# Performance work log

Measured on AMD Instinct MI355X. Metric: run time of the kernel, lower is better.

The kernel has to match this reference:

```python
import jax, jax.numpy as jnp
import numpy as np

CUTOFF = 5.0
COULOMB_CONSTANT = 14.3996454784936  # eV * Angstrom / e^2
SQRT2 = 1.4142135623730951
N_NODES = 500000
N_EDGES = 16000000


def polynomial_cutoff(r, cutoff):
    ratio = r / cutoff
    f = 1.0 - 6.0 * ratio**5 + 15.0 * ratio**4 - 10.0 * ratio**3
    return jnp.where(r <= cutoff, f, 0.0)


def setup_inputs() -> dict:
    key = jax.random.key(0)
    k1, k2, k3, k4, k5 = jax.random.split(key, 5)
    charge = jax.random.normal(k1, (N_NODES,), dtype=jnp.float32)
    # sigma in (0.5, 1.5): positive Gaussian widths
    sigma = jax.random.uniform(k2, (N_NODES,), dtype=jnp.float32) + 0.5
    # bond_dist in (0.1, CUTOFF)
    bond_dist = jax.random.uniform(k3, (N_EDGES,), dtype=jnp.float32) * (CUTOFF - 0.1) + 0.1
    src = jax.random.randint(k4, (N_EDGES,), 0, N_NODES, dtype=jnp.int32)
    dst = jax.random.randint(k5, (N_EDGES,), 0, N_NODES, dtype=jnp.int32)
    return {"charge": charge, "sigma": sigma, "bond_dist": bond_dist, "src": src, "dst": dst}


def reference(charge, sigma, bond_dist, src, dst):
    # Edge-wise message: q_dst * erf(r / (sqrt2 * gamma)) * fcut(r) / r * K
    gamma = jnp.sqrt(sigma[src] ** 2 + sigma[dst] ** 2)  # [E]
    msg = (
        charge[dst]
        * jax.scipy.special.erf(bond_dist / (SQRT2 * gamma))
        * polynomial_cutoff(bond_dist, CUTOFF)
        / bond_dist
    ) * COULOMB_CONSTANT
    # Sum-aggregate messages at destination nodes (DGL fn.sum semantics)
    elec_pot = jax.ops.segment_sum(msg, dst, num_segments=charge.shape[0])
    return elec_pot
```

## Files before the change

kernel.cpp:

```cpp
#include <hip/hip_runtime.h>
#include <hip/hip_fp16.h>
#include <math.h>
#include <stdint.h>

#define CUTOFF_F     5.0f
#define INV_CUTOFF   0.2f
#define KCOUL        14.3996454784936f
#define INV_SQRT2    0.7071067811865475f

typedef int            vint4    __attribute__((ext_vector_type(4)));
typedef float          vfloat4  __attribute__((ext_vector_type(4)));
typedef uint32_t       vuint4   __attribute__((ext_vector_type(4)));
typedef unsigned short vushort8 __attribute__((ext_vector_type(8)));

#define WSHIFT        11
#define WINDOW        2048
#define NB            245
#define EPT           8
#define EPB           4096
#define OFFS_STRIDE   256
#define SPAN_MAX      512

__device__ __forceinline__ float erf_approx(float x) {
    const float a1 = 0.254829592f, a2 = -0.284496736f, a3 = 1.421413741f,
                a4 = -1.453152027f, a5 = 1.061405429f, p = 0.3275911f;
    float t = __builtin_amdgcn_rcpf(fmaf(p, x, 1.0f));
    float poly = t * fmaf(t, fmaf(t, fmaf(t, fmaf(t, a5, a4), a3), a2), a1);
    return 1.0f - poly * __expf(-x * x);
}

__device__ __forceinline__ float edge_val(float rr, float s2sum) {
    float inv_gamma = rsqrtf(s2sum);
    float x  = rr * INV_CUTOFF;
    float fc = fmaf(x * x * x, fmaf(x, fmaf(-6.0f, x, 15.0f), -10.0f), 1.0f);
    fc = (rr <= CUTOFF_F) ? fc : 0.0f;
    return erf_approx(rr * INV_SQRT2 * inv_gamma) * fc * KCOUL
         * __builtin_amdgcn_rcpf(rr);
}

__global__ __launch_bounds__(256, 4) void p1_bin(
    const float* __restrict__ bond,
    const int*   __restrict__ src,
    const int*   __restrict__ dst,
    unsigned short* __restrict__ offs,
    uint32_t*       __restrict__ sl_out,
    unsigned short* __restrict__ r_out,
    int n_edges)
{
    __shared__ uint32_t hist[NB];
    __shared__ uint32_t scan_s[NB + 1];
    __shared__ alignas(16) uint32_t       buf_sl[EPB];
    __shared__ alignas(16) unsigned short buf_r[EPB];

    const int tid = threadIdx.x;
    const int e0  = blockIdx.x * EPB;

    if (tid < NB) hist[tid] = 0;
    __syncthreads();

    uint32_t slA[EPT], brA[EPT], slB[EPT], brB[EPT];
    unsigned short hrA[EPT], hrB[EPT];

    const bool full = (e0 + EPB <= n_edges);
    if (full) {
        {
            const vint4*   dp = (const vint4*)(dst + e0) + tid;
            const vint4*   sp = (const vint4*)(src + e0) + tid;
            const vfloat4* rp = (const vfloat4*)(bond + e0) + tid;
            vint4   d0 = __builtin_nontemporal_load(dp);
            vint4   d1 = __builtin_nontemporal_load(dp + 256);
            vint4   s0 = __builtin_nontemporal_load(sp);
            vint4   s1 = __builtin_nontemporal_load(sp + 256);
            vfloat4 r0 = __builtin_nontemporal_load(rp);
            vfloat4 r1 = __builtin_nontemporal_load(rp + 256);
            int   d[EPT] = {d0.x,d0.y,d0.z,d0.w,d1.x,d1.y,d1.z,d1.w};
            int   s[EPT] = {s0.x,s0.y,s0.z,s0.w,s1.x,s1.y,s1.z,s1.w};
            float r[EPT] = {r0.x,r0.y,r0.z,r0.w,r1.x,r1.y,r1.z,r1.w};
            #pragma unroll
            for (int j = 0; j < EPT; ++j) {
                unsigned b = (unsigned)d[j] >> WSHIFT;
                uint32_t rk = atomicAdd(&hist[b], 1u);
                brA[j] = (b << 16) | rk;
                slA[j] = ((uint32_t)s[j] << WSHIFT) | ((unsigned)d[j] & (WINDOW - 1));
                hrA[j] = __half_as_ushort(__float2half_rn(r[j]));
            }
        }
        {
            const vint4*   dp = (const vint4*)(dst + e0) + tid;
            const vint4*   sp = (const vint4*)(src + e0) + tid;
            const vfloat4* rp = (const vfloat4*)(bond + e0) + tid;
            vint4   d2 = __builtin_nontemporal_load(dp + 512);
            vint4   d3 = __builtin_nontemporal_load(dp + 768);
            vint4   s2 = __builtin_nontemporal_load(sp + 512);
            vint4   s3 = __builtin_nontemporal_load(sp + 768);
            vfloat4 r2 = __builtin_nontemporal_load(rp + 512);
            vfloat4 r3 = __builtin_nontemporal_load(rp + 768);
            int   d[EPT] = {d2.x,d2.y,d2.z,d2.w,d3.x,d3.y,d3.z,d3.w};
            int   s[EPT] = {s2.x,s2.y,s2.z,s2.w,s3.x,s3.y,s3.z,s3.w};
            float r[EPT] = {r2.x,r2.y,r2.z,r2.w,r3.x,r3.y,r3.z,r3.w};
            #pragma unroll
            for (int j = 0; j < EPT; ++j) {
                unsigned b = (unsigned)d[j] >> WSHIFT;
                uint32_t rk = atomicAdd(&hist[b], 1u);
                brB[j] = (b << 16) | rk;
                slB[j] = ((uint32_t)s[j] << WSHIFT) | ((unsigned)d[j] & (WINDOW - 1));
                hrB[j] = __half_as_ushort(__float2half_rn(r[j]));
            }
        }
    } else {
        #pragma unroll
        for (int j = 0; j < EPT; ++j) {
            int eA = e0 + (j >> 2) * 1024 + tid * 4 + (j & 3);
            int eB = eA + 2048;
            if (eA < n_edges) {
                int dv = dst[eA]; int sv = src[eA]; float rv = bond[eA];
                unsigned b = (unsigned)dv >> WSHIFT;
                uint32_t rk = atomicAdd(&hist[b], 1u);
                brA[j] = (b << 16) | rk;
                slA[j] = ((uint32_t)sv << WSHIFT) | ((unsigned)dv & (WINDOW - 1));
                hrA[j] = __half_as_ushort(__float2half_rn(rv));
            } else brA[j] = 0xFFFFFFFFu;
            if (eB < n_edges) {
                int dv = dst[eB]; int sv = src[eB]; float rv = bond[eB];
                unsigned b = (unsigned)dv >> WSHIFT;
                uint32_t rk = atomicAdd(&hist[b], 1u);
                brB[j] = (b << 16) | rk;
                slB[j] = ((uint32_t)sv << WSHIFT) | ((unsigned)dv & (WINDOW - 1));
                hrB[j] = __half_as_ushort(__float2half_rn(rv));
            } else brB[j] = 0xFFFFFFFFu;
        }
    }
    __syncthreads();

    if (tid < 64) {
        const int base = tid * 4;
        uint32_t v[4]; uint32_t s = 0;
        #pragma unroll
        for (int j = 0; j < 4; ++j) { v[j] = (base + j < NB) ? hist[base + j] : 0u; s += v[j]; }
        uint32_t inc = s;
        #pragma unroll
        for (int d = 1; d < 64; d <<= 1) {
            uint32_t up = __shfl_up(inc, d, 64);
            if (tid >= d) inc += up;
        }
        uint32_t excl = inc - s;
        #pragma unroll
        for (int j = 0; j < 4; ++j) {
            if (base + j <= NB) scan_s[base + j] = excl;
            excl += v[j];
        }
    }
    __syncthreads();

    #pragma unroll
    for (int j = 0; j < EPT; ++j)
        if (brA[j] != 0xFFFFFFFFu) {
            uint32_t p = scan_s[brA[j] >> 16] + (brA[j] & 0xFFFFu);
            buf_sl[p] = slA[j]; buf_r[p] = hrA[j];
        }
    #pragma unroll
    for (int j = 0; j < EPT; ++j)
        if (brB[j] != 0xFFFFFFFFu) {
            uint32_t p = scan_s[brB[j] >> 16] + (brB[j] & 0xFFFFu);
            buf_sl[p] = slB[j]; buf_r[p] = hrB[j];
        }
    __syncthreads();

    if (tid <= NB)
        offs[(size_t)blockIdx.x * OFFS_STRIDE + tid] = (unsigned short)scan_s[tid];

    {
        const vuint4* bs = (const vuint4*)buf_sl;
        vuint4* os = (vuint4*)(sl_out + (size_t)blockIdx.x * EPB);
        #pragma unroll
        for (int i = 0; i < EPB / 4 / 256; ++i)
            __builtin_nontemporal_store(bs[tid + i * 256], os + tid + i * 256);
        const vushort8* br = (const vushort8*)buf_r;
        vushort8* orr = (vushort8*)(r_out + (size_t)blockIdx.x * EPB);
        #pragma unroll
        for (int i = 0; i < EPB / 8 / 256; ++i)
            __builtin_nontemporal_store(br[tid + i * 256], orr + tid + i * 256);
    }
}

template<int WPB>
__global__ __launch_bounds__(256, 4) void p2_acc(
    const uint32_t*       __restrict__ sl_in,
    const unsigned short* __restrict__ r_in,
    const unsigned short* __restrict__ offs,
    const float*          __restrict__ sigma,
    float*                __restrict__ partials,
    int n_nodes, int nblk)
{
    __shared__ float acc[WINDOW];
    __shared__ float sig[WINDOW];
    __shared__ unsigned short offLo[SPAN_MAX];
    __shared__ uint32_t cum[SPAN_MAX + 1];

    const int g = blockIdx.x;
    const int b = g / WPB;
    const int w = g % WPB;

    vfloat4* accv = (vfloat4*)acc;
    for (int i = threadIdx.x; i < WINDOW / 4; i += 256)
        accv[i] = (vfloat4){0.f, 0.f, 0.f, 0.f};

    const int nbase  = b << WSHIFT;
    const int nvalid = (n_nodes - nbase < WINDOW) ? (n_nodes - nbase) : WINDOW;
    if (nvalid == WINDOW) {
        vfloat4* sv = (vfloat4*)sig;
        const vfloat4* gp = (const vfloat4*)(sigma + nbase);
        for (int i = threadIdx.x; i < WINDOW / 4; i += 256) sv[i] = gp[i];
    } else {
        for (int i = threadIdx.x; i < WINDOW; i += 256)
            sig[i] = (i < nvalid) ? sigma[nbase + i] : 0.f;
    }

    const int span = (nblk + WPB - 1) / WPB;
    const int blk0 = w * span;
    int blkN = nblk - blk0;
    if (blkN > span) blkN = span;
    if (blkN < 0) blkN = 0;
    for (int i = threadIdx.x; i < blkN; i += 256) {
        size_t o = (size_t)(blk0 + i) * OFFS_STRIDE + b;
        unsigned short lo = offs[o];
        offLo[i] = lo;
        cum[i] = (uint32_t)offs[o + 1] - lo;
    }
    __syncthreads();

    if (threadIdx.x < 64) {
        const int base = threadIdx.x * 8;
        uint32_t v[8]; uint32_t s = 0;
        #pragma unroll
        for (int j = 0; j < 8; ++j) { v[j] = (base + j < blkN) ? cum[base + j] : 0u; s += v[j]; }
        uint32_t inc = s;
        #pragma unroll
        for (int d = 1; d < 64; d <<= 1) {
            uint32_t up = __shfl_up(inc, d, 64);
            if (threadIdx.x >= d) inc += up;
        }
        uint32_t excl = inc - s;
        #pragma unroll
        for (int j = 0; j < 8; ++j) { uint32_t t = v[j]; cum[base + j] = excl; excl += t; }
        if (threadIdx.x == 63) cum[SPAN_MAX] = inc;
    }
    __syncthreads();

    const int wave = threadIdx.x >> 6, lane = threadIdx.x & 63;
    const uint32_t T = cum[blkN];

    const uint32_t chunk = (T + 3) >> 2;
    const uint32_t f0    = (uint32_t)wave * chunk;
    uint32_t fend        = f0 + chunk;
    if (fend > T) fend = T;

    if (f0 < fend) {
        int l = 0, r = blkN;
        while (l < r) {
            int m = (l + r) >> 1;
            if (cum[m + 1] <= f0) l = m + 1; else r = m;
        }
        int i = l;

        for (uint32_t fb = f0; fb < fend; fb += 64) {
            uint32_t f = fb + lane;
            int ii = i;
            if (f < fend) {
                while (cum[ii + 1] <= f) ++ii;
                uint32_t k = f - cum[ii];
                size_t addr = (size_t)(blk0 + ii) * EPB + offLo[ii] + k;
                uint32_t sl = sl_in[addr];
                float rr = __half2float(__ushort_as_half(r_in[addr]));
                float ss = sigma[sl >> WSHIFT];
                float sd = sig[sl & (WINDOW - 1)];
                float v  = edge_val(rr, fmaf(ss, ss, sd * sd));
                atomicAdd(&acc[sl & (WINDOW - 1)], v);
            }
            i = __shfl(ii, 63);
        }
    }
    __syncthreads();

    vfloat4* outp = (vfloat4*)(partials + (size_t)g * WINDOW);
    for (int i = threadIdx.x; i < WINDOW / 4; i += 256)
        __builtin_nontemporal_store(accv[i], outp + i);
}

template<int WPB>
__global__ __launch_bounds__(256) void p3_reduce(
    const float* __restrict__ partials,
    const float* __restrict__ charge,
    float*       __restrict__ out, int n_nodes)
{
    int n = blockIdx.x * 256 + threadIdx.x;
    if (n >= n_nodes) return;
    unsigned b     = (unsigned)n >> WSHIFT;
    unsigned local = (unsigned)n & (WINDOW - 1);
    const float* p = partials + ((size_t)b * WPB) * WINDOW + local;
    float sum = 0.0f;
    #pragma unroll
    for (int w = 0; w < WPB; ++w)
        sum += __builtin_nontemporal_load(p + (size_t)w * WINDOW);
    out[n] = charge[n] * sum;
}

__global__ __launch_bounds__(256) void edge_msg_atomic(
    const float* __restrict__ charge, const float* __restrict__ sigma,
    const float* __restrict__ bond, const int* __restrict__ src,
    const int* __restrict__ dst, float* __restrict__ out, int n_edges)
{
    int i = blockIdx.x * blockDim.x + threadIdx.x;
    if (i < n_edges) {
        float ss = sigma[src[i]], sd = sigma[dst[i]];
        float msg = charge[dst[i]] * edge_val(bond[i], fmaf(ss, ss, sd * sd));
        atomicAdd(&out[dst[i]], msg);
    }
}

extern "C" void kernel_launch(void* const* d_in, const int* in_sizes, int n_in,
                              void* d_out, int out_size, void* d_ws, size_t ws_size,
                              hipStream_t stream) {
    const float* charge = (const float*)d_in[0];
    const float* sigma  = (const float*)d_in[1];
    const float* bond   = (const float*)d_in[2];
    const int*   src    = (const int*)d_in[3];
    const int*   dst    = (const int*)d_in[4];
    float* out = (float*)d_out;

    int n_nodes = in_sizes[0];
    int n_edges = in_sizes[2];

    int nblk = (n_edges + EPB - 1) / EPB;

    size_t offs_b = (size_t)nblk * OFFS_STRIDE * sizeof(unsigned short);
    size_t sl_b   = (size_t)nblk * EPB * sizeof(uint32_t);
    size_t r_b    = (size_t)nblk * EPB * sizeof(unsigned short);
    size_t base_b = offs_b + sl_b + r_b;

    int wpb = 0;
    {
        size_t p16 = (size_t)NB * 16 * WINDOW * sizeof(float);
        size_t p8  = (size_t)NB * 8  * WINDOW * sizeof(float);
        int span16 = (nblk + 15) / 16, span8 = (nblk + 7) / 8;
        if (base_b + p16 <= ws_size && span16 <= SPAN_MAX) wpb = 16;
        else if (base_b + p8 <= ws_size && span8 <= SPAN_MAX) wpb = 8;
    }

    if (n_nodes <= NB * WINDOW && wpb != 0) {
        unsigned short* offs = (unsigned short*)d_ws;
        uint32_t*       slp  = (uint32_t*)((char*)d_ws + offs_b);
        unsigned short* rp   = (unsigned short*)((char*)d_ws + offs_b + sl_b);
        float* partial = (float*)((char*)d_ws + base_b);

        p1_bin<<<nblk, 256, 0, stream>>>(bond, src, dst, offs, slp, rp, n_edges);
        int blocks3 = (n_nodes + 255) / 256;
        if (wpb == 16) {
            p2_acc<16><<<NB * 16, 256, 0, stream>>>(slp, rp, offs, sigma, partial,
                                                    n_nodes, nblk);
            p3_reduce<16><<<blocks3, 256, 0, stream>>>(partial, charge, out, n_nodes);
        } else {
            p2_acc<8><<<NB * 8, 256, 0, stream>>>(slp, rp, offs, sigma, partial,
                                                  n_nodes, nblk);
            p3_reduce<8><<<blocks3, 256, 0, stream>>>(partial, charge, out, n_nodes);
        }
    } else {
        (void)hipMemsetAsync(out, 0, (size_t)n_nodes * sizeof(float), stream);
        int blocks = (n_edges + 255) / 256;
        edge_msg_atomic<<<blocks, 256, 0, stream>>>(charge, sigma, bond, src, dst,
                                                    out, n_edges);
    }
}
```

Baseline: 327.6 us.

## Compute edge messages in binning pass and store packed fp16 value records

The edge message (erf, cutoff, 1/r) is now computed in the binning kernel, which gathers sigma for both src and dst there. Each edge is stored as a single 32-bit record holding the local dst index and the message in fp16, replacing the separate src/dst word and fp16 distance. The accumulate kernel no longer loads sigma windows or does random sigma[src] gathers; it only reads records and does LDS atomics. This cuts intermediate traffic and p2's scattered gathers, at the cost of random dst-sigma gathers in p1 and fp16 rounding of the message value instead of the distance.

```diff
diff --git a/kernel.cpp b/kernel.cpp
--- a/kernel.cpp
+++ b/kernel.cpp
@@ -11,7 +11,6 @@
 typedef int            vint4    __attribute__((ext_vector_type(4)));
 typedef float          vfloat4  __attribute__((ext_vector_type(4)));
 typedef uint32_t       vuint4   __attribute__((ext_vector_type(4)));
-typedef unsigned short vushort8 __attribute__((ext_vector_type(8)));
 
 #define WSHIFT        11
 #define WINDOW        2048
@@ -38,19 +37,30 @@
          * __builtin_amdgcn_rcpf(rr);
 }
 
+__device__ __forceinline__ void pack_edge(
+    int dv, int sv_unused, float rv, float ss, float sd,
+    uint32_t* hist, uint32_t& br, uint32_t& rec)
+{
+    unsigned b = (unsigned)dv >> WSHIFT;
+    uint32_t rk = atomicAdd(&hist[b], 1u);
+    br = (b << 16) | rk;
+    float v = edge_val(rv, fmaf(ss, ss, sd * sd));
+    rec = ((uint32_t)((unsigned)dv & (WINDOW - 1)) << 16)
+        | (uint32_t)__half_as_ushort(__float2half_rn(v));
+}
+
 __global__ __launch_bounds__(256, 4) void p1_bin(
     const float* __restrict__ bond,
     const int*   __restrict__ src,
     const int*   __restrict__ dst,
+    const float* __restrict__ sigma,
     unsigned short* __restrict__ offs,
-    uint32_t*       __restrict__ sl_out,
-    unsigned short* __restrict__ r_out,
+    uint32_t*       __restrict__ rec_out,
     int n_edges)
 {
     __shared__ uint32_t hist[NB];
     __shared__ uint32_t scan_s[NB + 1];
-    __shared__ alignas(16) uint32_t       buf_sl[EPB];
-    __shared__ alignas(16) unsigned short buf_r[EPB];
+    __shared__ alignas(16) uint32_t buf[EPB];
 
     const int tid = threadIdx.x;
     const int e0  = blockIdx.x * EPB;
@@ -58,8 +68,7 @@
     if (tid < NB) hist[tid] = 0;
     __syncthreads();
 
-    uint32_t slA[EPT], brA[EPT], slB[EPT], brB[EPT];
-    unsigned short hrA[EPT], hrB[EPT];
+    uint32_t recA[EPT], brA[EPT], recB[EPT], brB[EPT];
 
     const bool full = (e0 + EPB <= n_edges);
     if (full) {
@@ -76,14 +85,12 @@
             int   d[EPT] = {d0.x,d0.y,d0.z,d0.w,d1.x,d1.y,d1.z,d1.w};
             int   s[EPT] = {s0.x,s0.y,s0.z,s0.w,s1.x,s1.y,s1.z,s1.w};
             float r[EPT] = {r0.x,r0.y,r0.z,r0.w,r1.x,r1.y,r1.z,r1.w};
+            float ss[EPT], sd[EPT];
             #pragma unroll
-            for (int j = 0; j < EPT; ++j) {
-                unsigned b = (unsigned)d[j] >> WSHIFT;
-                uint32_t rk = atomicAdd(&hist[b], 1u);
-                brA[j] = (b << 16) | rk;
-                slA[j] = ((uint32_t)s[j] << WSHIFT) | ((unsigned)d[j] & (WINDOW - 1));
-                hrA[j] = __half_as_ushort(__float2half_rn(r[j]));
-            }
+            for (int j = 0; j < EPT; ++j) { ss[j] = sigma[s[j]]; sd[j] = sigma[d[j]]; }
+            #pragma unroll
+            for (int j = 0; j < EPT; ++j)
+                pack_edge(d[j], s[j], r[j], ss[j], sd[j], hist, brA[j], recA[j]);
         }
         {
             const vint4*   dp = (const vint4*)(dst + e0) + tid;
@@ -98,14 +105,12 @@
             int   d[EPT] = {d2.x,d2.y,d2.z,d2.w,d3.x,d3.y,d3.z,d3.w};
             int   s[EPT] = {s2.x,s2.y,s2.z,s2.w,s3.x,s3.y,s3.z,s3.w};
             float r[EPT] = {r2.x,r2.y,r2.z,r2.w,r3.x,r3.y,r3.z,r3.w};
+            float ss[EPT], sd[EPT];
             #pragma unroll
-            for (int j = 0; j < EPT; ++j) {
-                unsigned b = (unsigned)d[j] >> WSHIFT;
-                uint32_t rk = atomicAdd(&hist[b], 1u);
-                brB[j] = (b << 16) | rk;
-                slB[j] = ((uint32_t)s[j] << WSHIFT) | ((unsigned)d[j] & (WINDOW - 1));
-                hrB[j] = __half_as_ushort(__float2half_rn(r[j]));
-            }
+            for (int j = 0; j < EPT; ++j) { ss[j] = sigma[s[j]]; sd[j] = sigma[d[j]]; }
+            #pragma unroll
+            for (int j = 0; j < EPT; ++j)
+                pack_edge(d[j], s[j], r[j], ss[j], sd[j], hist, brB[j], recB[j]);
         }
     } else {
         #pragma unroll
@@ -114,19 +119,11 @@
             int eB = eA + 2048;
             if (eA < n_edges) {
                 int dv = dst[eA]; int sv = src[eA]; float rv = bond[eA];
-                unsigned b = (unsigned)dv >> WSHIFT;
-                uint32_t rk = atomicAdd(&hist[b], 1u);
-                brA[j] = (b << 16) | rk;
-                slA[j] = ((uint32_t)sv << WSHIFT) | ((unsigned)dv & (WINDOW - 1));
-                hrA[j] = __half_as_ushort(__float2half_rn(rv));
+                pack_edge(dv, sv, rv, sigma[sv], sigma[dv], hist, brA[j], recA[j]);
             } else brA[j] = 0xFFFFFFFFu;
             if (eB < n_edges) {
                 int dv = dst[eB]; int sv = src[eB]; float rv = bond[eB];
-                unsigned b = (unsigned)dv >> WSHIFT;
-                uint32_t rk = atomicAdd(&hist[b], 1u);
-                brB[j] = (b << 16) | rk;
-                slB[j] = ((uint32_t)sv << WSHIFT) | ((unsigned)dv & (WINDOW - 1));
-                hrB[j] = __half_as_ushort(__float2half_rn(rv));
+                pack_edge(dv, sv, rv, sigma[sv], sigma[dv], hist, brB[j], recB[j]);
             } else brB[j] = 0xFFFFFFFFu;
         }
     }
@@ -154,46 +151,34 @@
 
     #pragma unroll
     for (int j = 0; j < EPT; ++j)
-        if (brA[j] != 0xFFFFFFFFu) {
-            uint32_t p = scan_s[brA[j] >> 16] + (brA[j] & 0xFFFFu);
-            buf_sl[p] = slA[j]; buf_r[p] = hrA[j];
-        }
+        if (brA[j] != 0xFFFFFFFFu)
+            buf[scan_s[brA[j] >> 16] + (brA[j] & 0xFFFFu)] = recA[j];
     #pragma unroll
     for (int j = 0; j < EPT; ++j)
-        if (brB[j] != 0xFFFFFFFFu) {
-            uint32_t p = scan_s[brB[j] >> 16] + (brB[j] & 0xFFFFu);
-            buf_sl[p] = slB[j]; buf_r[p] = hrB[j];
-        }
+        if (brB[j] != 0xFFFFFFFFu)
+            buf[scan_s[brB[j] >> 16] + (brB[j] & 0xFFFFu)] = recB[j];
     __syncthreads();
 
     if (tid <= NB)
         offs[(size_t)blockIdx.x * OFFS_STRIDE + tid] = (unsigned short)scan_s[tid];
 
     {
-        const vuint4* bs = (const vuint4*)buf_sl;
-        vuint4* os = (vuint4*)(sl_out + (size_t)blockIdx.x * EPB);
+        const vuint4* bs = (const vuint4*)buf;
+        vuint4* os = (vuint4*)(rec_out + (size_t)blockIdx.x * EPB);
         #pragma unroll
         for (int i = 0; i < EPB / 4 / 256; ++i)
             __builtin_nontemporal_store(bs[tid + i * 256], os + tid + i * 256);
-        const vushort8* br = (const vushort8*)buf_r;
-        vushort8* orr = (vushort8*)(r_out + (size_t)blockIdx.x * EPB);
-        #pragma unroll
-        for (int i = 0; i < EPB / 8 / 256; ++i)
-            __builtin_nontemporal_store(br[tid + i * 256], orr + tid + i * 256);
     }
 }
 
 template<int WPB>
 __global__ __launch_bounds__(256, 4) void p2_acc(
-    const uint32_t*       __restrict__ sl_in,
-    const unsigned short* __restrict__ r_in,
+    const uint32_t*       __restrict__ rec_in,
     const unsigned short* __restrict__ offs,
-    const float*          __restrict__ sigma,
     float*                __restrict__ partials,
     int n_nodes, int nblk)
 {
     __shared__ float acc[WINDOW];
-    __shared__ float sig[WINDOW];
     __shared__ unsigned short offLo[SPAN_MAX];
     __shared__ uint32_t cum[SPAN_MAX + 1];
 
@@ -204,17 +189,6 @@
     vfloat4* accv = (vfloat4*)acc;
     for (int i = threadIdx.x; i < WINDOW / 4; i += 256)
         accv[i] = (vfloat4){0.f, 0.f, 0.f, 0.f};
-
-    const int nbase  = b << WSHIFT;
-    const int nvalid = (n_nodes - nbase < WINDOW) ? (n_nodes - nbase) : WINDOW;
-    if (nvalid == WINDOW) {
-        vfloat4* sv = (vfloat4*)sig;
-        const vfloat4* gp = (const vfloat4*)(sigma + nbase);
-        for (int i = threadIdx.x; i < WINDOW / 4; i += 256) sv[i] = gp[i];
-    } else {
-        for (int i = threadIdx.x; i < WINDOW; i += 256)
-            sig[i] = (i < nvalid) ? sigma[nbase + i] : 0.f;
-    }
 
     const int span = (nblk + WPB - 1) / WPB;
     const int blk0 = w * span;
@@ -270,12 +244,9 @@
                 while (cum[ii + 1] <= f) ++ii;
                 uint32_t k = f - cum[ii];
                 size_t addr = (size_t)(blk0 + ii) * EPB + offLo[ii] + k;
-                uint32_t sl = sl_in[addr];
-                float rr = __half2float(__ushort_as_half(r_in[addr]));
-                float ss = sigma[sl >> WSHIFT];
-                float sd = sig[sl & (WINDOW - 1)];
-                float v  = edge_val(rr, fmaf(ss, ss, sd * sd));
-                atomicAdd(&acc[sl & (WINDOW - 1)], v);
+                uint32_t rec = rec_in[addr];
+                float v = __half2float(__ushort_as_half((unsigned short)rec));
+                atomicAdd(&acc[rec >> 16], v);
             }
             i = __shfl(ii, 63);
         }
@@ -334,9 +305,8 @@
     int nblk = (n_edges + EPB - 1) / EPB;
 
     size_t offs_b = (size_t)nblk * OFFS_STRIDE * sizeof(unsigned short);
-    size_t sl_b   = (size_t)nblk * EPB * sizeof(uint32_t);
-    size_t r_b    = (size_t)nblk * EPB * sizeof(unsigned short);
-    size_t base_b = offs_b + sl_b + r_b;
+    size_t rec_b  = (size_t)nblk * EPB * sizeof(uint32_t);
+    size_t base_b = offs_b + rec_b;
 
     int wpb = 0;
     {
@@ -349,18 +319,18 @@
 
     if (n_nodes <= NB * WINDOW && wpb != 0) {
         unsigned short* offs = (unsigned short*)d_ws;
-        uint32_t*       slp  = (uint32_t*)((char*)d_ws + offs_b);
-        unsigned short* rp   = (unsigned short*)((char*)d_ws + offs_b + sl_b);
+        uint32_t*       recp = (uint32_t*)((char*)d_ws + offs_b);
         float* partial = (float*)((char*)d_ws + base_b);
 
-        p1_bin<<<nblk, 256, 0, stream>>>(bond, src, dst, offs, slp, rp, n_edges);
+        p1_bin<<<nblk, 256, 0, stream>>>(bond, src, dst, sigma, offs, recp,
+                                         n_edges);
         int blocks3 = (n_nodes + 255) / 256;
         if (wpb == 16) {
-            p2_acc<16><<<NB * 16, 256, 0, stream>>>(slp, rp, offs, sigma, partial,
+            p2_acc<16><<<NB * 16, 256, 0, stream>>>(recp, offs, partial,
                                                     n_nodes, nblk);
             p3_reduce<16><<<blocks3, 256, 0, stream>>>(partial, charge, out, n_nodes);
         } else {
-            p2_acc<8><<<NB * 8, 256, 0, stream>>>(slp, rp, offs, sigma, partial,
+            p2_acc<8><<<NB * 8, 256, 0, stream>>>(recp, offs, partial,
                                                   n_nodes, nblk);
             p3_reduce<8><<<blocks3, 256, 0, stream>>>(partial, charge, out, n_nodes);
         }
```

After: 403.7 us. 1.23x slower.

## Precompute per-edge run IDs in LDS and batch four edge loads per thread

Applied to the files above, without the earlier changes.

The accumulation kernel now builds a shared-memory table that maps each flattened edge index to its source block, using one binary search per entry. It also precomputes a base address per block, which replaces the per-lane linear walk and the wave shuffle. The edge loop then has each thread issue four independent global loads before computing, to expose more memory-level parallelism. Entries beyond a fixed table capacity fall back to a per-edge binary search. The cost is extra LDS (run-ID table, base array), which may reduce occupancy, plus an extra barrier and setup pass.

```diff
diff --git a/kernel.cpp b/kernel.cpp
--- a/kernel.cpp
+++ b/kernel.cpp
@@ -19,7 +19,6 @@
 #define EPT           8
 #define EPB           4096
 #define OFFS_STRIDE   256
-#define SPAN_MAX      512
 
 __device__ __forceinline__ float erf_approx(float x) {
     const float a1 = 0.254829592f, a2 = -0.284496736f, a3 = 1.421413741f,
@@ -183,7 +182,7 @@
     }
 }
 
-template<int WPB>
+template<int WPB, typename RID, int T_MAX, int SPAN_CAP>
 __global__ __launch_bounds__(256, 4) void p2_acc(
     const uint32_t*       __restrict__ sl_in,
     const unsigned short* __restrict__ r_in,
@@ -194,8 +193,9 @@
 {
     __shared__ float acc[WINDOW];
     __shared__ float sig[WINDOW];
-    __shared__ unsigned short offLo[SPAN_MAX];
-    __shared__ uint32_t cum[SPAN_MAX + 1];
+    __shared__ uint32_t cum[SPAN_CAP + 1];
+    __shared__ uint32_t baseA[SPAN_CAP];
+    __shared__ RID      runID[T_MAX];
 
     const int g = blockIdx.x;
     const int b = g / WPB;
@@ -223,17 +223,18 @@
     if (blkN < 0) blkN = 0;
     for (int i = threadIdx.x; i < blkN; i += 256) {
         size_t o = (size_t)(blk0 + i) * OFFS_STRIDE + b;
-        unsigned short lo = offs[o];
-        offLo[i] = lo;
-        cum[i] = (uint32_t)offs[o + 1] - lo;
+        uint32_t lo = offs[o];
+        cum[i]   = (uint32_t)offs[o + 1] - lo;
+        baseA[i] = (uint32_t)(blk0 + i) * EPB + lo;
     }
     __syncthreads();
 
     if (threadIdx.x < 64) {
-        const int base = threadIdx.x * 8;
-        uint32_t v[8]; uint32_t s = 0;
-        #pragma unroll
-        for (int j = 0; j < 8; ++j) { v[j] = (base + j < blkN) ? cum[base + j] : 0u; s += v[j]; }
+        constexpr int EL = SPAN_CAP / 64;
+        const int base = threadIdx.x * EL;
+        uint32_t v[EL]; uint32_t s = 0;
+        #pragma unroll
+        for (int j = 0; j < EL; ++j) { v[j] = (base + j < blkN) ? cum[base + j] : 0u; s += v[j]; }
         uint32_t inc = s;
         #pragma unroll
         for (int d = 1; d < 64; d <<= 1) {
@@ -242,43 +243,66 @@
         }
         uint32_t excl = inc - s;
         #pragma unroll
-        for (int j = 0; j < 8; ++j) { uint32_t t = v[j]; cum[base + j] = excl; excl += t; }
-        if (threadIdx.x == 63) cum[SPAN_MAX] = inc;
-    }
-    __syncthreads();
-
-    const int wave = threadIdx.x >> 6, lane = threadIdx.x & 63;
-    const uint32_t T = cum[blkN];
-
-    const uint32_t chunk = (T + 3) >> 2;
-    const uint32_t f0    = (uint32_t)wave * chunk;
-    uint32_t fend        = f0 + chunk;
-    if (fend > T) fend = T;
-
-    if (f0 < fend) {
+        for (int j = 0; j < EL; ++j) { uint32_t t = v[j]; cum[base + j] = excl; excl += t; }
+        if (threadIdx.x == 63) cum[SPAN_CAP] = inc;
+    }
+    __syncthreads();
+
+    const uint32_t T  = cum[blkN];
+    const uint32_t Tc = (T < (uint32_t)T_MAX) ? T : (uint32_t)T_MAX;
+
+    for (int i = threadIdx.x; i < blkN; i += 256) baseA[i] -= cum[i];
+    for (uint32_t p = threadIdx.x; p < Tc; p += 256) {
         int l = 0, r = blkN;
         while (l < r) {
             int m = (l + r) >> 1;
-            if (cum[m + 1] <= f0) l = m + 1; else r = m;
-        }
-        int i = l;
-
-        for (uint32_t fb = f0; fb < fend; fb += 64) {
-            uint32_t f = fb + lane;
-            int ii = i;
-            if (f < fend) {
-                while (cum[ii + 1] <= f) ++ii;
-                uint32_t k = f - cum[ii];
-                size_t addr = (size_t)(blk0 + ii) * EPB + offLo[ii] + k;
-                uint32_t sl = sl_in[addr];
-                float rr = __half2float(__ushort_as_half(r_in[addr]));
-                float ss = sigma[sl >> WSHIFT];
-                float sd = sig[sl & (WINDOW - 1)];
-                float v  = edge_val(rr, fmaf(ss, ss, sd * sd));
-                atomicAdd(&acc[sl & (WINDOW - 1)], v);
-            }
-            i = __shfl(ii, 63);
-        }
+            if (cum[m + 1] <= p) l = m + 1; else r = m;
+        }
+        runID[p] = (RID)l;
+    }
+    __syncthreads();
+
+    for (uint32_t f0 = threadIdx.x; f0 < Tc; f0 += 1024u) {
+        uint32_t sl4[4]; unsigned short rh4[4]; bool ok[4];
+        #pragma unroll
+        for (int j = 0; j < 4; ++j) {
+            uint32_t f = f0 + (uint32_t)j * 256u;
+            ok[j] = (f < Tc);
+            if (ok[j]) {
+                uint32_t a = baseA[runID[f]] + f;
+                sl4[j] = sl_in[a];
+                rh4[j] = r_in[a];
+            }
+        }
+        float ss4[4], sd4[4];
+        #pragma unroll
+        for (int j = 0; j < 4; ++j)
+            if (ok[j]) {
+                ss4[j] = sigma[sl4[j] >> WSHIFT];
+                sd4[j] = sig[sl4[j] & (WINDOW - 1)];
+            }
+        #pragma unroll
+        for (int j = 0; j < 4; ++j)
+            if (ok[j]) {
+                float rr = __half2float(__ushort_as_half(rh4[j]));
+                float v  = edge_val(rr, fmaf(ss4[j], ss4[j], sd4[j] * sd4[j]));
+                atomicAdd(&acc[sl4[j] & (WINDOW - 1)], v);
+            }
+    }
+
+    for (uint32_t f = (uint32_t)T_MAX + threadIdx.x; f < T; f += 256u) {
+        int l = 0, r = blkN;
+        while (l < r) {
+            int m = (l + r) >> 1;
+            if (cum[m + 1] <= f) l = m + 1; else r = m;
+        }
+        uint32_t a = baseA[l] + f;
+        uint32_t sl = sl_in[a];
+        float rr = __half2float(__ushort_as_half(r_in[a]));
+        float ss = sigma[sl >> WSHIFT];
+        float sd = sig[sl & (WINDOW - 1)];
+        float v  = edge_val(rr, fmaf(ss, ss, sd * sd));
+        atomicAdd(&acc[sl & (WINDOW - 1)], v);
     }
     __syncthreads();
 
@@ -343,8 +367,8 @@
         size_t p16 = (size_t)NB * 16 * WINDOW * sizeof(float);
         size_t p8  = (size_t)NB * 8  * WINDOW * sizeof(float);
         int span16 = (nblk + 15) / 16, span8 = (nblk + 7) / 8;
-        if (base_b + p16 <= ws_size && span16 <= SPAN_MAX) wpb = 16;
-        else if (base_b + p8 <= ws_size && span8 <= SPAN_MAX) wpb = 8;
+        if (base_b + p16 <= ws_size && span16 <= 256) wpb = 16;
+        else if (base_b + p8 <= ws_size && span8 <= 512) wpb = 8;
     }
 
     if (n_nodes <= NB * WINDOW && wpb != 0) {
@@ -356,12 +380,14 @@
         p1_bin<<<nblk, 256, 0, stream>>>(bond, src, dst, offs, slp, rp, n_edges);
         int blocks3 = (n_nodes + 255) / 256;
         if (wpb == 16) {
-            p2_acc<16><<<NB * 16, 256, 0, stream>>>(slp, rp, offs, sigma, partial,
-                                                    n_nodes, nblk);
+            p2_acc<16, unsigned char, 6144, 256>
+                <<<NB * 16, 256, 0, stream>>>(slp, rp, offs, sigma, partial,
+                                              n_nodes, nblk);
             p3_reduce<16><<<blocks3, 256, 0, stream>>>(partial, charge, out, n_nodes);
         } else {
-            p2_acc<8><<<NB * 8, 256, 0, stream>>>(slp, rp, offs, sigma, partial,
-                                                  n_nodes, nblk);
+            p2_acc<8, unsigned short, 10240, 512>
+                <<<NB * 8, 256, 0, stream>>>(slp, rp, offs, sigma, partial,
+                                             n_nodes, nblk);
             p3_reduce<8><<<blocks3, 256, 0, stream>>>(partial, charge, out, n_nodes);
         }
     } else {
```

After: 337.5 us. 1.03x slower.
